# Kernel optimization log

Hardware: AMD Instinct MI355X
Metric: run time of the kernel (lower is better)

The kernel has to match this reference:

```python
import jax, jax.numpy as jnp
import numpy as np

BN = 1.0 / np.sqrt(1.0 + 1e-5)  # eval-mode BatchNorm at init (mean=0,var=1,gamma=1,beta=0)
EPS = 1e-5
WIN = 5
NH, HD = 8, 6

def _conv2d(x, w, ph, pw, groups=1):
    return jax.lax.conv_general_dilated(x, w, (1, 1), ((ph, ph), (pw, pw)),
        dimension_numbers=('NCHW', 'OIHW', 'NCHW'), feature_group_count=groups)

def _conv1d(x, w, p, groups=1):
    return jax.lax.conv_general_dilated(x, w, (1,), ((p, p),),
        dimension_numbers=('NCH', 'OIH', 'NCH'), feature_group_count=groups)

def _avgpool_t(x, k):
    s = jax.lax.reduce_window(x, 0.0, jax.lax.add, (1, 1, 1, k), (1, 1, 1, k), 'VALID')
    return s / k

def _ln(h, g, b):
    m = h.mean(-1, keepdims=True)
    v = h.var(-1, keepdims=True)  # biased, matches torch LayerNorm
    return (h - m) / jnp.sqrt(v + EPS) * g + b

def setup_inputs() -> dict:
    ks = jax.random.split(jax.random.key(0), 20)
    def n(i, shape, s=0.05):
        return jax.random.normal(ks[i], shape, dtype=jnp.float32) * s
    z = lambda *s: jnp.zeros(s, jnp.float32)
    o = lambda *s: jnp.ones(s, jnp.float32)
    return {
        'x': jax.random.normal(ks[0], (16, 1, 22, 16000), dtype=jnp.float32),
        'riem_w1': n(1, (253, 256)), 'riem_b1': z(256),
        'riem_w2': n(2, (256, 48)), 'riem_b2': z(48),
        'conv1_w': n(3, (16, 1, 1, 64)),
        'dw1_w': n(4, (32, 1, 22, 1)),
        'dw2_w': n(5, (32, 1, 1, 16)),
        'pw_w': n(6, (48, 32, 1, 1)),
        'tc1_w': n(7, (24, 2, 3)), 'tc1_b': z(24),
        'tc2_w': n(8, (48, 24, 1)), 'tc2_b': z(48),
        'fusion_proj': n(9, (48, 48), 0.15),
        'pos_enc': n(10, (1, 500, 48), 0.02),
        'ln1_g': o(4, 48), 'ln1_b': z(4, 48),
        'qkv_w': n(11, (4, 48, 144)), 'qkv_b': z(4, 144),
        'attn_proj_w': n(12, (4, 48, 48)), 'attn_proj_b': z(4, 48),
        'ln2_g': o(4, 48), 'ln2_b': z(4, 48),
        'ffn_w1': n(13, (4, 48, 192)), 'ffn_b1': z(4, 192),
        'ffn_w2': n(14, (4, 192, 48)), 'ffn_b2': z(4, 48),
        'cls_ln_g': o(48), 'cls_ln_b': z(48),
        'cls_w': n(15, (48, 4), 0.1), 'cls_b': z(4),
    }

def _forward(x, riem_w1, riem_b1, riem_w2, riem_b2, conv1_w, dw1_w, dw2_w, pw_w,
             tc1_w, tc1_b, tc2_w, tc2_b, fusion_proj, pos_enc,
             ln1_g, ln1_b, qkv_w, qkv_b, attn_proj_w, attn_proj_b,
             ln2_g, ln2_b, ffn_w1, ffn_b1, ffn_w2, ffn_b2,
             cls_ln_g, cls_ln_b, cls_w, cls_b):
    B = x.shape[0]
    # ---- Riemannian geometry branch ----
    xr = x[:, 0]                                   # (B, 22, T)
    C, T = xr.shape[1], xr.shape[2]
    xc = xr - xr.mean(-1, keepdims=True)
    cov = jnp.einsum('bct,bdt->bcd', xc, xc) / (T - 1)
    I = jnp.eye(C, dtype=x.dtype)
    cov = cov + I * 1e-5
    tr = jnp.trace(cov, axis1=1, axis2=2)
    cov = cov + I * (tr.mean() * 1e-3)
    L = jnp.linalg.cholesky(cov)
    dL = jnp.diagonal(L, axis1=-2, axis2=-1)
    log_cov = L * jnp.log(jnp.clip(dL, 1e-10))[:, None, :]   # L @ diag(log(diag L))
    iu = jnp.triu_indices(C)
    flat = log_cov[:, iu[0], iu[1]]                # (B, 253)
    r_feat = (jax.nn.elu(flat @ riem_w1 + riem_b1) @ riem_w2 + riem_b2)[:, None, :]
    # ---- Lightweight CNN branch (BatchNorms in eval = constant scale) ----
    h = _conv2d(x, conv1_w, 0, 32) * BN
    h = jax.nn.elu(_conv2d(h, dw1_w, 0, 0, groups=16) * BN)
    h = _avgpool_t(h, 8)
    h = _conv2d(h, dw2_w, 0, 8, groups=32) * BN
    h = jax.nn.elu(_conv2d(h, pw_w, 0, 0) * BN)
    h = _avgpool_t(h, 8)                            # (B, 48, 1, L)
    feat = jnp.transpose(h[:, :, 0, :], (0, 2, 1))  # (B, L, 48)
    t = _conv1d(jnp.transpose(feat, (0, 2, 1)), tc1_w, 1, groups=24) + tc1_b[None, :, None]
    t = jax.nn.gelu(t * BN, approximate=False)
    t = _conv1d(t, tc2_w, 0) + tc2_b[None, :, None]
    feat = feat + jnp.transpose(t, (0, 2, 1))
    # ---- Fusion + positional encoding ----
    fused = jnp.concatenate([r_feat, feat], axis=1) @ fusion_proj
    N = fused.shape[1]
    fused = fused + pos_enc[:, :N]
    # ---- Sparse (banded) transformer blocks ----
    idx = jnp.arange(N)
    band = jnp.abs(idx[:, None] - idx[None, :]) <= WIN   # allowed positions
    scale = HD ** -0.5
    for i in range(4):
        res = fused
        hh = _ln(fused, ln1_g[i], ln1_b[i])
        qkv = (hh @ qkv_w[i] + qkv_b[i]).reshape(B, N, 3, NH, HD)
        q = jnp.transpose(qkv[:, :, 0], (0, 2, 1, 3))
        k = jnp.transpose(qkv[:, :, 1], (0, 2, 1, 3))
        v = jnp.transpose(qkv[:, :, 2], (0, 2, 1, 3))
        att = jnp.einsum('bhqd,bhkd->bhqk', q, k) * scale
        att = jax.nn.softmax(jnp.where(band, att, -jnp.inf), axis=-1)
        o = jnp.einsum('bhqk,bhkd->bhqd', att, v)
        o = jnp.transpose(o, (0, 2, 1, 3)).reshape(B, N, NH * HD)
        fused = res + (o @ attn_proj_w[i] + attn_proj_b[i])
        res = fused
        hh = _ln(fused, ln2_g[i], ln2_b[i])
        hh = jax.nn.gelu(hh @ ffn_w1[i] + ffn_b1[i], approximate=False) @ ffn_w2[i] + ffn_b2[i]
        fused = res + hh
    g = fused.mean(axis=1)
    g = _ln(g, cls_ln_g, cls_ln_b)
    return g @ cls_w + cls_b

def reference(x, riem_w1, riem_b1, riem_w2, riem_b2, conv1_w, dw1_w, dw2_w, pw_w,
              tc1_w, tc1_b, tc2_w, tc2_b, fusion_proj, pos_enc,
              ln1_g, ln1_b, qkv_w, qkv_b, attn_proj_w, attn_proj_b,
              ln2_g, ln2_b, ffn_w1, ffn_b1, ffn_w2, ffn_b2,
              cls_ln_g, cls_ln_b, cls_w, cls_b):
    return _forward(x, riem_w1, riem_b1, riem_w2, riem_b2, conv1_w, dw1_w, dw2_w, pw_w,
                    tc1_w, tc1_b, tc2_w, tc2_b, fusion_proj, pos_enc,
                    ln1_g, ln1_b, qkv_w, qkv_b, attn_proj_w, attn_proj_b,
                    ln2_g, ln2_b, ffn_w1, ffn_b1, ffn_w2, ffn_b2,
                    cls_ln_g, cls_ln_b, cls_w, cls_b)
```

## Files before the change

### kernel.cpp

```cpp
#include <hip/hip_runtime.h>
#include <hip/hip_bf16.h>
#include <math.h>

#define BN_C 0.9999950000375f
#define NB 16
#define NC 22
#define NT 16000
#define NPAIR 253
#define NSEQ 251
#define ND 48
#define TR 8
#define TE 18

__device__ __forceinline__ unsigned short f2bf(float f) {
    union { float f; unsigned int u; } v; v.f = f;
    unsigned int r = v.u + 0x7fff + ((v.u >> 16) & 1);
    return (unsigned short)(r >> 16);
}
__device__ __forceinline__ float bf2f(unsigned short s) {
    union { unsigned int u; float f; } v; v.u = ((unsigned int)s) << 16;
    return v.f;
}

__global__ __launch_bounds__(256) void k_y(const float* __restrict__ x,
                                           const float* __restrict__ dw1,
                                           __hip_bfloat16* __restrict__ y) {
    int gid = blockIdx.x * 256 + threadIdx.x;
    int b = gid / 8000, tp = gid % 8000;
    int t = tp * 2;
    const float* xb = x + (size_t)b * NC * NT + t;
    float a0[32], a1[32];
    #pragma unroll
    for (int j = 0; j < 32; j++) { a0[j] = 0.f; a1[j] = 0.f; }
    for (int h = 0; h < NC; h++) {
        float2 xv = *(const float2*)&xb[(size_t)h * NT];
        #pragma unroll
        for (int j = 0; j < 32; j++) {
            float w = dw1[j * NC + h];
            a0[j] += w * xv.x; a1[j] += w * xv.y;
        }
    }
    unsigned int* yo = (unsigned int*)(y + (size_t)b * 32 * NT + t);
    #pragma unroll
    for (int j = 0; j < 32; j++) {
        unsigned int pk = (unsigned int)f2bf(a0[j]) | ((unsigned int)f2bf(a1[j]) << 16);
        yo[j * (NT / 2)] = pk;
    }
}

#define TCHUNK 500
#define XROW 504
__global__ __launch_bounds__(256) void k_covS(const float* __restrict__ x,
                                              float* __restrict__ covP,
                                              float* __restrict__ sumP) {
    int chunk = blockIdx.x, b = blockIdx.y;
    int t0 = chunk * TCHUNK;
    __shared__ unsigned short xs[NC * XROW];
    const float* xp = x + (size_t)b * NC * NT + t0;
    for (int i = threadIdx.x; i < NC * 126; i += 256) {
        int c = i / 126, q = i % 126;
        unsigned long long pk = 0ull;
        if (q < 125) {
            float4 v = *(const float4*)&xp[(size_t)c * NT + 4 * q];
            pk = (unsigned long long)f2bf(v.x) | ((unsigned long long)f2bf(v.y) << 16)
               | ((unsigned long long)f2bf(v.z) << 32) | ((unsigned long long)f2bf(v.w) << 48);
        }
        *(unsigned long long*)&xs[c * XROW + 4 * q] = pk;
    }
    __syncthreads();
    int p = threadIdx.x;
    if (p < NPAIR) {
        int c = 0, r = p;
        while (r >= NC - c) { r -= NC - c; c++; }
        int d = c + r;
        const unsigned short* xc = &xs[c * XROW];
        const unsigned short* xd = &xs[d * XROW];
        float a0 = 0, a1 = 0, a2 = 0, a3 = 0;
        float s0 = 0, s1 = 0, s2 = 0, s3 = 0;
        for (int t = 0; t < XROW; t += 8) {
            uint4 pc = *(const uint4*)&xc[t];
            uint4 pd = *(const uint4*)&xd[t];
            float c0 = bf2f((unsigned short)pc.x), c1 = bf2f((unsigned short)(pc.x >> 16));
            float c2 = bf2f((unsigned short)pc.y), c3 = bf2f((unsigned short)(pc.y >> 16));
            float c4 = bf2f((unsigned short)pc.z), c5 = bf2f((unsigned short)(pc.z >> 16));
            float c6 = bf2f((unsigned short)pc.w), c7 = bf2f((unsigned short)(pc.w >> 16));
            float d0 = bf2f((unsigned short)pd.x), d1 = bf2f((unsigned short)(pd.x >> 16));
            float d2 = bf2f((unsigned short)pd.y), d3 = bf2f((unsigned short)(pd.y >> 16));
            float d4 = bf2f((unsigned short)pd.z), d5 = bf2f((unsigned short)(pd.z >> 16));
            float d6 = bf2f((unsigned short)pd.w), d7 = bf2f((unsigned short)(pd.w >> 16));
            a0 += c0 * d0 + c4 * d4; a1 += c1 * d1 + c5 * d5;
            a2 += c2 * d2 + c6 * d6; a3 += c3 * d3 + c7 * d7;
            s0 += c0 + c4; s1 += c1 + c5; s2 += c2 + c6; s3 += c3 + c7;
        }
        covP[(size_t)chunk * NB * NPAIR + b * NPAIR + p] = (a0 + a1) + (a2 + a3);
        if (c == d) sumP[(size_t)chunk * NB * NC + b * NC + c] = (s0 + s1) + (s2 + s3);
    }
}

__global__ void k_cov_asm(const float* __restrict__ covP, const float* __restrict__ sumP,
                          float* __restrict__ cov, float* __restrict__ trb) {
    int b = blockIdx.x, t = threadIdx.x;
    __shared__ float ss[NC];
    __shared__ float red[256];
    if (t < NC) {
        float s = 0;
        for (int ch = 0; ch < 32; ch++) s += sumP[(size_t)ch * NB * NC + b * NC + t];
        ss[t] = s;
    }
    __syncthreads();
    float myTr = 0.f;
    if (t < NPAIR) {
        int c = 0, r = t;
        while (r >= NC - c) { r -= NC - c; c++; }
        int d = c + r;
        float v = 0;
        for (int ch = 0; ch < 32; ch++) v += covP[(size_t)ch * NB * NPAIR + b * NPAIR + t];
        v = (v - ss[c] * ss[d] / (float)NT) / (float)(NT - 1);
        if (c == d) { v += 1e-5f; myTr = v; }
        cov[b * 484 + c * NC + d] = v;
        cov[b * 484 + d * NC + c] = v;
    }
    red[t] = myTr;
    __syncthreads();
    for (int st = 128; st > 0; st >>= 1) {
        if (t < st) red[t] += red[t + st];
        __syncthreads();
    }
    if (t == 0) trb[b] = red[0];
}

__global__ __launch_bounds__(256) void k_cholfeat(
    const float* __restrict__ cov, const float* __restrict__ trb,
    const float* __restrict__ w1, const float* __restrict__ b1,
    const float* __restrict__ w2, const float* __restrict__ b2,
    float* __restrict__ rfeat) {
    int b = blockIdx.x, t = threadIdx.x;
    __shared__ float dvs[NC];
    __shared__ float hid[256];
    __shared__ float part[4][ND];
    if (t < 64) {
        int lane = t;
        float tv = (lane < NB) ? trb[lane] : 0.f;
        tv += __shfl_down(tv, 8, 16); tv += __shfl_down(tv, 4, 16);
        tv += __shfl_down(tv, 2, 16); tv += __shfl_down(tv, 1, 16);
        float trm = __shfl(tv, 0) * (0.001f / (float)NB);
        float a[NC];
        #pragma unroll
        for (int j = 0; j < NC; j++) {
            float v = (lane < NC) ? cov[b * 484 + lane * NC + j] : 0.f;
            a[j] = v + ((j == lane) ? trm : 0.f);
        }
        float diagv = 1.f;
        #pragma unroll
        for (int k = 0; k < NC; k++) {
            float akk = __shfl(a[k], k);
            float dk = sqrtf(akk);
            if (lane == k) { a[k] = dk; diagv = dk; }
            else if (lane > k) a[k] /= dk;
            float myak = a[k];
            #pragma unroll
            for (int j = k + 1; j < NC; j++) {
                float ljk = __shfl(myak, j);
                if (lane >= j) a[j] -= myak * ljk;
            }
        }
        if (lane < NC) dvs[lane] = diagv * logf(fmaxf(diagv, 1e-10f));
    }
    __syncthreads();
    {
        float acc = b1[t];
        #pragma unroll
        for (int d = 0; d < NC; d++) {
            int pos = d * NC - d * (d - 1) / 2;
            acc += dvs[d] * w1[pos * 256 + t];
        }
        hid[t] = (acc > 0.f) ? acc : expm1f(acc);
    }
    __syncthreads();
    if (t < 192) {
        int col = t % ND, kc = t / ND;
        float a = 0.f;
        #pragma unroll
        for (int i = 0; i < 64; i++) a += hid[kc * 64 + i] * w2[(kc * 64 + i) * ND + col];
        part[kc][col] = a;
    }
    __syncthreads();
    if (t < ND)
        rfeat[b * ND + t] = b2[t] + part[0][t] + part[1][t] + part[2][t] + part[3][t];
}

#define UT 256
__global__ __launch_bounds__(256) void k_conv64(const __hip_bfloat16* __restrict__ y,
                                                const float* __restrict__ c1w,
                                                float* __restrict__ p) {
    int tile = blockIdx.x, j = blockIdx.y, b = blockIdx.z;
    int u0 = tile * UT;
    __shared__ float yt[2376];
    const __hip_bfloat16* yp = y + ((size_t)(b * 32 + j)) * NT;
    int tbase = u0 * 8 - 32;
    for (int q = threadIdx.x; q < 1056; q += 256) {
        int i = 2 * q;
        int tq = tbase + i;
        float v0 = 0.f, v1 = 0.f;
        if (tq >= 0 && tq + 1 < NT) {
            unsigned int pk = *(const unsigned int*)(yp + tq);
            v0 = bf2f((unsigned short)pk); v1 = bf2f((unsigned short)(pk >> 16));
        } else {
            if (tq >= 0 && tq < NT) v0 = __bfloat162float(yp[tq]);
            if (tq + 1 >= 0 && tq + 1 < NT) v1 = __bfloat162float(yp[tq + 1]);
        }
        yt[i + (i >> 3)] = v0;
        int i1 = i + 1;
        yt[i1 + (i1 >> 3)] = v1;
    }
    __syncthreads();
    const float* cf = c1w + (j >> 1) * 64;
    int u = u0 + threadIdx.x;
    if (u < 2000) {
        int off = 8 * threadIdx.x;
        float acc[8];
        #pragma unroll
        for (int s = 0; s < 8; s++) acc[s] = 0.f;
        #pragma unroll
        for (int kb = 0; kb < 64; kb += 16) {
            float Yb[23];
            #pragma unroll
            for (int m = 0; m < 23; m++) {
                int idx = off + kb + m;
                Yb[m] = yt[idx + (idx >> 3)];
            }
            #pragma unroll
            for (int k = 0; k < 16; k++) {
                float c = cf[kb + k];
                #pragma unroll
                for (int s = 0; s < 8; s++) acc[s] += c * Yb[k + s];
            }
        }
        const float bn2 = BN_C * BN_C;
        float pv = 0.f;
        #pragma unroll
        for (int s = 0; s < 8; s++) {
            float z = bn2 * acc[s];
            pv += (z > 0.f) ? z : expm1f(z);
        }
        p[((size_t)(b * 32 + j)) * 2000 + u] = pv * 0.125f;
    }
}

__global__ __launch_bounds__(256) void k_stage2(const float* __restrict__ p,
                                                const float* __restrict__ dw2,
                                                const float* __restrict__ pw,
                                                float* __restrict__ feat) {
    int u2b = blockIdx.x * 4, b = blockIdx.y, t = threadIdx.x;
    __shared__ float pt[32][48];
    __shared__ float dval[32][32];
    __shared__ float w2s[512];
    __shared__ float pws[1536];
    for (int i = t; i < 512; i += 256) w2s[i] = dw2[i];
    for (int i = t; i < 1536; i += 256) pws[i] = pw[i];
    int base = 8 * u2b - 8;
    for (int i = t; i < 32 * 47; i += 256) {
        int j = i / 47, tt = i % 47;
        int gt = base + tt;
        pt[j][tt] = (gt >= 0 && gt < 2000) ? p[((size_t)(b * 32 + j)) * 2000 + gt] : 0.f;
    }
    __syncthreads();
    for (int i = t; i < 1024; i += 256) {
        int j = i >> 5, su = i & 31;
        int u = su >> 3, s = su & 7;
        float a = 0.f;
        #pragma unroll
        for (int k = 0; k < 16; k++) a += w2s[j * 16 + k] * pt[j][8 * u + s + k];
        dval[j][su] = a * BN_C;
    }
    __syncthreads();
    if (t < 192) {
        int col = t % ND, u = t / ND;
        int u2 = u2b + u;
        if (u2 < 250) {
            float wreg[32];
            #pragma unroll
            for (int j = 0; j < 32; j++) wreg[j] = pws[col * 32 + j];
            float acc = 0.f;
            #pragma unroll
            for (int s = 0; s < 8; s++) {
                float e = 0.f;
                #pragma unroll
                for (int j = 0; j < 32; j++) e += wreg[j] * dval[j][u * 8 + s];
                e *= BN_C;
                acc += (e > 0.f) ? e : expm1f(e);
            }
            feat[((size_t)b * 250 + u2) * ND + col] = acc * 0.125f;
        }
    }
}

__global__ __launch_bounds__(256) void k_fuse(
    const float* __restrict__ feat, const float* __restrict__ rfeat,
    const float* __restrict__ tc1w, const float* __restrict__ tc1b,
    const float* __restrict__ tc2w, const float* __restrict__ tc2b,
    const float* __restrict__ fp, const float* __restrict__ pe,
    float* __restrict__ fused) {
    int b = blockIdx.y;
    int sub = threadIdx.x >> 6, lt = threadIdx.x & 63;
    int n = blockIdx.x * 4 + sub;
    bool valid = (n < NSEQ);
    __shared__ float row[4][ND];
    __shared__ float g1[4][24];
    if (valid) {
        if (n == 0) {
            if (lt < ND) row[sub][lt] = rfeat[b * ND + lt];
        } else {
            int u = n - 1;
            if (lt < 24) {
                int m = lt;
                float a = tc1b[m];
                #pragma unroll
                for (int k = 0; k < 3; k++) {
                    int uu = u + k - 1;
                    if (uu >= 0 && uu < 250) {
                        float f0 = feat[((size_t)b * 250 + uu) * ND + 2 * m];
                        float f1 = feat[((size_t)b * 250 + uu) * ND + 2 * m + 1];
                        a += tc1w[m * 6 + k] * f0 + tc1w[m * 6 + 3 + k] * f1;
                    }
                }
                float z = a * BN_C;
                g1[sub][m] = 0.5f * z * (1.f + erff(z * 0.70710678f));
            }
        }
    }
    __syncthreads();
    if (valid && n > 0 && lt < ND) {
        int u = n - 1;
        float a = tc2b[lt];
        #pragma unroll
        for (int m = 0; m < 24; m++) a += tc2w[lt * 24 + m] * g1[sub][m];
        row[sub][lt] = feat[((size_t)b * 250 + u) * ND + lt] + a;
    }
    __syncthreads();
    if (valid && lt < ND) {
        float o = pe[n * ND + lt];
        for (int c = 0; c < ND; c++) o += row[sub][c] * fp[c * ND + lt];
        fused[((size_t)b * NSEQ + n) * ND + lt] = o;
    }
}

__global__ __launch_bounds__(512) void k_layer(
    float* __restrict__ fused,
    const float* __restrict__ g1v, const float* __restrict__ b1v,
    const float* __restrict__ qw, const float* __restrict__ qb,
    const float* __restrict__ apw, const float* __restrict__ apb,
    const float* __restrict__ g2v, const float* __restrict__ b2v,
    const float* __restrict__ w1, const float* __restrict__ fb1,
    const float* __restrict__ w2, const float* __restrict__ fb2) {
    int tile = blockIdx.x, b = blockIdx.y;
    int n0 = tile * TR;
    int t = threadIdx.x;
    __shared__ float row[TE][ND];
    __shared__ float hh[TE][ND];
    __shared__ float qkvS[TE * 144];
    __shared__ float ob[TR][ND];
    __shared__ float nrow[TR][ND];
    __shared__ float mrs[TE][2];
    __shared__ float part[4][TR][ND];
    float* hid = qkvS;

    for (int i = t; i < TE * ND; i += 512) {
        int e = i / ND, c = i % ND;
        int n = n0 - 5 + e;
        row[e][c] = (n >= 0 && n < NSEQ) ? fused[((size_t)b * NSEQ + n) * ND + c] : 0.f;
    }
    __syncthreads();
    if (t < TE * 16) {
        int r = t >> 4, i = t & 15;
        float v0 = row[r][i], v1 = row[r][i + 16], v2 = row[r][i + 32];
        float s = v0 + v1 + v2;
        s += __shfl_down(s, 8, 16); s += __shfl_down(s, 4, 16);
        s += __shfl_down(s, 2, 16); s += __shfl_down(s, 1, 16);
        float m = __shfl(s, 0, 16) * (1.f / ND);
        float d0 = v0 - m, d1 = v1 - m, d2 = v2 - m;
        float q = d0 * d0 + d1 * d1 + d2 * d2;
        q += __shfl_down(q, 8, 16); q += __shfl_down(q, 4, 16);
        q += __shfl_down(q, 2, 16); q += __shfl_down(q, 1, 16);
        if (i == 0) { mrs[r][0] = m; mrs[r][1] = rsqrtf(q * (1.f / ND) + 1e-5f); }
    }
    __syncthreads();
    for (int i = t; i < TE * ND; i += 512) {
        int e = i / ND, c = i % ND;
        hh[e][c] = (row[e][c] - mrs[e][0]) * mrs[e][1] * g1v[c] + b1v[c];
    }
    __syncthreads();
    if (t < 288) {
        int col = t % 144, eg = t / 144;
        float w[ND];
        #pragma unroll
        for (int c = 0; c < ND; c++) w[c] = qw[c * 144 + col];
        float bias = qb[col];
        for (int e = eg * 9; e < eg * 9 + 9; e++) {
            float a = bias;
            #pragma unroll
            for (int c = 0; c < ND; c++) a += hh[e][c] * w[c];
            qkvS[e * 144 + col] = a;
        }
    }
    __syncthreads();
    if (t < TR * 8) {
        int r = t >> 3, h = t & 7;
        int n = n0 + r;
        if (n < NSEQ) {
            int k0 = n - 5; if (k0 < 0) k0 = 0;
            int k1 = n + 5; if (k1 > NSEQ - 1) k1 = NSEQ - 1;
            int nk = k1 - k0 + 1;
            float q[6];
            #pragma unroll
            for (int d = 0; d < 6; d++) q[d] = qkvS[(r + 5) * 144 + h * 6 + d];
            float sc[11];
            float mx = -1e30f;
            for (int ki = 0; ki < nk; ki++) {
                int e = k0 + ki - n0 + 5;
                float s = 0;
                #pragma unroll
                for (int d = 0; d < 6; d++) s += q[d] * qkvS[e * 144 + 48 + h * 6 + d];
                s *= 0.4082482904638631f;
                sc[ki] = s; mx = fmaxf(mx, s);
            }
            float sum = 0;
            for (int ki = 0; ki < nk; ki++) { float e = expf(sc[ki] - mx); sc[ki] = e; sum += e; }
            float inv = 1.f / sum;
            float o[6] = {0, 0, 0, 0, 0, 0};
            for (int ki = 0; ki < nk; ki++) {
                int e = k0 + ki - n0 + 5;
                float pv = sc[ki] * inv;
                #pragma unroll
                for (int d = 0; d < 6; d++) o[d] += pv * qkvS[e * 144 + 96 + h * 6 + d];
            }
            #pragma unroll
            for (int d = 0; d < 6; d++) ob[r][h * 6 + d] = o[d];
        } else {
            #pragma unroll
            for (int d = 0; d < 6; d++) ob[r][h * 6 + d] = 0.f;
        }
    }
    __syncthreads();
    if (t < TR * ND) {
        int r = t / ND, col = t % ND;
        float a = apb[col];
        #pragma unroll
        for (int c = 0; c < ND; c++) a += ob[r][c] * apw[c * ND + col];
        nrow[r][col] = row[r + 5][col] + a;
    }
    __syncthreads();
    if (t < TR * 16) {
        int r = t >> 4, i = t & 15;
        float v0 = nrow[r][i], v1 = nrow[r][i + 16], v2 = nrow[r][i + 32];
        float s = v0 + v1 + v2;
        s += __shfl_down(s, 8, 16); s += __shfl_down(s, 4, 16);
        s += __shfl_down(s, 2, 16); s += __shfl_down(s, 1, 16);
        float m = __shfl(s, 0, 16) * (1.f / ND);
        float d0 = v0 - m, d1 = v1 - m, d2 = v2 - m;
        float q = d0 * d0 + d1 * d1 + d2 * d2;
        q += __shfl_down(q, 8, 16); q += __shfl_down(q, 4, 16);
        q += __shfl_down(q, 2, 16); q += __shfl_down(q, 1, 16);
        if (i == 0) { mrs[r][0] = m; mrs[r][1] = rsqrtf(q * (1.f / ND) + 1e-5f); }
    }
    __syncthreads();
    if (t < TR * ND) {
        int r = t / ND, c = t % ND;
        hh[r][c] = (nrow[r][c] - mrs[r][0]) * mrs[r][1] * g2v[c] + b2v[c];
    }
    __syncthreads();
    if (t < 384) {
        int col = t % 192, rg = t / 192;
        float w[ND];
        #pragma unroll
        for (int c = 0; c < ND; c++) w[c] = w1[c * 192 + col];
        float bias = fb1[col];
        for (int r = rg * 4; r < rg * 4 + 4; r++) {
            float a = bias;
            #pragma unroll
            for (int c = 0; c < ND; c++) a += hh[r][c] * w[c];
            hid[r * 192 + col] = 0.5f * a * (1.f + erff(a * 0.70710678f));
        }
    }
    __syncthreads();
    if (t < 384) {
        int col = t % ND, kc = (t / ND) & 3, rh = t / 192;
        float w[ND];
        #pragma unroll
        for (int i2 = 0; i2 < ND; i2++) w[i2] = w2[(kc * ND + i2) * ND + col];
        for (int r = rh * 4; r < rh * 4 + 4; r++) {
            float a = 0;
            #pragma unroll
            for (int i2 = 0; i2 < ND; i2++) a += hid[r * 192 + kc * ND + i2] * w[i2];
            part[kc][r][col] = a;
        }
    }
    __syncthreads();
    for (int i = t; i < TR * ND; i += 512) {
        int r = i / ND, c = i % ND;
        int n = n0 + r;
        if (n < NSEQ) {
            fused[((size_t)b * NSEQ + n) * ND + c] =
                nrow[r][c] + fb2[c] + part[0][r][c] + part[1][r][c] + part[2][r][c] + part[3][r][c];
        }
    }
}

__global__ void k_head(const float* __restrict__ fused, const float* __restrict__ lg,
                       const float* __restrict__ lb, const float* __restrict__ cw,
                       const float* __restrict__ cb, float* __restrict__ out) {
    int b = blockIdx.x, t = threadIdx.x;
    __shared__ float part[4][ND];
    __shared__ float gg[ND], mv[2];
    if (t < 192) {
        int col = t % ND, qt = t / ND;
        int nA = qt * 63;
        int nB = (nA + 63 < NSEQ) ? nA + 63 : NSEQ;
        float s = 0.f;
        for (int n = nA; n < nB; n++) s += fused[((size_t)b * NSEQ + n) * ND + col];
        part[qt][col] = s;
    }
    __syncthreads();
    if (t < ND) gg[t] = (part[0][t] + part[1][t] + part[2][t] + part[3][t]) * (1.f / NSEQ);
    __syncthreads();
    if (t == 0) {
        float m = 0;
        for (int c = 0; c < ND; c++) m += gg[c];
        m /= (float)ND;
        float v = 0;
        for (int c = 0; c < ND; c++) { float dd = gg[c] - m; v += dd * dd; }
        v /= (float)ND;
        mv[0] = m; mv[1] = rsqrtf(v + 1e-5f);
    }
    __syncthreads();
    if (t < ND) gg[t] = (gg[t] - mv[0]) * mv[1] * lg[t] + lb[t];
    __syncthreads();
    if (t < 4) {
        float a = cb[t];
        for (int c = 0; c < ND; c++) a += gg[c] * cw[c * 4 + t];
        out[b * 4 + t] = a;
    }
}

extern "C" void kernel_launch(void* const* d_in, const int* in_sizes, int n_in,
                              void* d_out, int out_size, void* d_ws, size_t ws_size,
                              hipStream_t stream) {
    const float* x       = (const float*)d_in[0];
    const float* riem_w1 = (const float*)d_in[1];
    const float* riem_b1 = (const float*)d_in[2];
    const float* riem_w2 = (const float*)d_in[3];
    const float* riem_b2 = (const float*)d_in[4];
    const float* conv1_w = (const float*)d_in[5];
    const float* dw1_w   = (const float*)d_in[6];
    const float* dw2_w   = (const float*)d_in[7];
    const float* pw_w    = (const float*)d_in[8];
    const float* tc1_w   = (const float*)d_in[9];
    const float* tc1_b   = (const float*)d_in[10];
    const float* tc2_w   = (const float*)d_in[11];
    const float* tc2_b   = (const float*)d_in[12];
    const float* fusion  = (const float*)d_in[13];
    const float* pos_enc = (const float*)d_in[14];
    const float* ln1_g   = (const float*)d_in[15];
    const float* ln1_b   = (const float*)d_in[16];
    const float* qkv_w   = (const float*)d_in[17];
    const float* qkv_b   = (const float*)d_in[18];
    const float* apw     = (const float*)d_in[19];
    const float* apb     = (const float*)d_in[20];
    const float* ln2_g   = (const float*)d_in[21];
    const float* ln2_b   = (const float*)d_in[22];
    const float* ffn_w1  = (const float*)d_in[23];
    const float* ffn_b1  = (const float*)d_in[24];
    const float* ffn_w2  = (const float*)d_in[25];
    const float* ffn_b2  = (const float*)d_in[26];
    const float* cls_g   = (const float*)d_in[27];
    const float* cls_b_  = (const float*)d_in[28];
    const float* cls_w   = (const float*)d_in[29];
    const float* cls_bb  = (const float*)d_in[30];
    float* out = (float*)d_out;

    float* ws = (float*)d_ws;
    float* covP  = ws;
    float* sumP  = ws + 129536;
    float* trb   = ws + 140800;
    float* cov   = ws + 140816;
    float* rfeat = ws + 148560;
    float* feat  = ws + 149328;
    float* fused = ws + 341328;
    float* pbuf  = ws + 534096;
    __hip_bfloat16* ybuf = (__hip_bfloat16*)(ws + 1558096);

    k_y<<<500, 256, 0, stream>>>(x, dw1_w, ybuf);
    k_covS<<<dim3(32, NB), 256, 0, stream>>>(x, covP, sumP);
    k_cov_asm<<<NB, 256, 0, stream>>>(covP, sumP, cov, trb);
    k_cholfeat<<<NB, 256, 0, stream>>>(cov, trb, riem_w1, riem_b1, riem_w2, riem_b2, rfeat);

    k_conv64<<<dim3(8, 32, NB), 256, 0, stream>>>(ybuf, conv1_w, pbuf);
    k_stage2<<<dim3(63, NB), 256, 0, stream>>>(pbuf, dw2_w, pw_w, feat);
    k_fuse<<<dim3(63, NB), 256, 0, stream>>>(feat, rfeat, tc1_w, tc1_b, tc2_w, tc2_b,
                                             fusion, pos_enc, fused);

    for (int i = 0; i < 4; i++) {
        k_layer<<<dim3(32, NB), 512, 0, stream>>>(
            fused, ln1_g + i * 48, ln1_b + i * 48, qkv_w + i * 6912, qkv_b + i * 144,
            apw + i * 2304, apb + i * 48, ln2_g + i * 48, ln2_b + i * 48,
            ffn_w1 + i * 9216, ffn_b1 + i * 192, ffn_w2 + i * 9216, ffn_b2 + i * 48);
    }

    k_head<<<NB, 256, 0, stream>>>(fused, cls_g, cls_b_, cls_w, cls_bb, out);
}
```

Before: 294.6 us.

## Fuse covariance assembly into Cholesky and stage2 into fuse; widen conv64 tiles

Folds covariance assembly and the trace reduction into the Cholesky-feature kernel. Each block recomputes the cross-batch trace from the partial sums, so no separate kernel or global round trip is needed. Merges stage2 and the fuse kernel: each block computes a 6-row halo of features in shared memory instead of writing and rereading a feature buffer. Doubles conv64 outputs per thread, halving the block count, to improve register reuse of the loaded inputs. These remove two launches and some global traffic, at the cost of redundant halo and trace work plus higher register pressure in conv64.

```diff
diff --git a/kernel.cpp b/kernel.cpp
--- a/kernel.cpp
+++ b/kernel.cpp
@@ -97,57 +97,55 @@
     }
 }
 
-__global__ void k_cov_asm(const float* __restrict__ covP, const float* __restrict__ sumP,
-                          float* __restrict__ cov, float* __restrict__ trb) {
+__global__ __launch_bounds__(256) void k_cholfeat(
+    const float* __restrict__ covP, const float* __restrict__ sumP,
+    const float* __restrict__ w1, const float* __restrict__ b1,
+    const float* __restrict__ w2, const float* __restrict__ b2,
+    float* __restrict__ rfeat) {
     int b = blockIdx.x, t = threadIdx.x;
-    __shared__ float ss[NC];
-    __shared__ float red[256];
-    if (t < NC) {
-        float s = 0;
-        for (int ch = 0; ch < 32; ch++) s += sumP[(size_t)ch * NB * NC + b * NC + t];
-        ss[t] = s;
-    }
-    __syncthreads();
-    float myTr = 0.f;
+    __shared__ float ssA[NB][NC];
+    __shared__ float covL[484];
+    __shared__ float trS[NB];
+    __shared__ float dvs[NC];
+    __shared__ float hid[256];
+    __shared__ float part[4][ND];
+    if (t < NB) trS[t] = 0.f;
+    for (int i = t; i < NB * NC; i += 256) {
+        int bb = i / NC, c = i % NC;
+        float s = 0.f;
+        for (int ch = 0; ch < 32; ch++) s += sumP[(size_t)ch * NB * NC + bb * NC + c];
+        ssA[bb][c] = s;
+    }
+    __syncthreads();
     if (t < NPAIR) {
         int c = 0, r = t;
         while (r >= NC - c) { r -= NC - c; c++; }
         int d = c + r;
-        float v = 0;
+        float v = 0.f;
         for (int ch = 0; ch < 32; ch++) v += covP[(size_t)ch * NB * NPAIR + b * NPAIR + t];
-        v = (v - ss[c] * ss[d] / (float)NT) / (float)(NT - 1);
-        if (c == d) { v += 1e-5f; myTr = v; }
-        cov[b * 484 + c * NC + d] = v;
-        cov[b * 484 + d * NC + c] = v;
-    }
-    red[t] = myTr;
-    __syncthreads();
-    for (int st = 128; st > 0; st >>= 1) {
-        if (t < st) red[t] += red[t + st];
-        __syncthreads();
-    }
-    if (t == 0) trb[b] = red[0];
-}
-
-__global__ __launch_bounds__(256) void k_cholfeat(
-    const float* __restrict__ cov, const float* __restrict__ trb,
-    const float* __restrict__ w1, const float* __restrict__ b1,
-    const float* __restrict__ w2, const float* __restrict__ b2,
-    float* __restrict__ rfeat) {
-    int b = blockIdx.x, t = threadIdx.x;
-    __shared__ float dvs[NC];
-    __shared__ float hid[256];
-    __shared__ float part[4][ND];
+        v = (v - ssA[b][c] * ssA[b][d] / (float)NT) / (float)(NT - 1);
+        if (c == d) v += 1e-5f;
+        covL[c * NC + d] = v;
+        covL[d * NC + c] = v;
+    }
+    for (int i = t; i < NB * NC; i += 256) {
+        int bb = i / NC, c = i % NC;
+        int pos = c * NC - c * (c - 1) / 2;
+        float v = 0.f;
+        for (int ch = 0; ch < 32; ch++) v += covP[(size_t)ch * NB * NPAIR + bb * NPAIR + pos];
+        v = (v - ssA[bb][c] * ssA[bb][c] / (float)NT) / (float)(NT - 1) + 1e-5f;
+        atomicAdd(&trS[bb], v);
+    }
+    __syncthreads();
+    float trs = 0.f;
+    for (int i = 0; i < NB; i++) trs += trS[i];
+    float trm = trs * (0.001f / (float)NB);
     if (t < 64) {
         int lane = t;
-        float tv = (lane < NB) ? trb[lane] : 0.f;
-        tv += __shfl_down(tv, 8, 16); tv += __shfl_down(tv, 4, 16);
-        tv += __shfl_down(tv, 2, 16); tv += __shfl_down(tv, 1, 16);
-        float trm = __shfl(tv, 0) * (0.001f / (float)NB);
         float a[NC];
         #pragma unroll
         for (int j = 0; j < NC; j++) {
-            float v = (lane < NC) ? cov[b * 484 + lane * NC + j] : 0.f;
+            float v = (lane < NC) ? covL[lane * NC + j] : 0.f;
             a[j] = v + ((j == lane) ? trm : 0.f);
         }
         float diagv = 1.f;
@@ -189,16 +187,16 @@
         rfeat[b * ND + t] = b2[t] + part[0][t] + part[1][t] + part[2][t] + part[3][t];
 }
 
-#define UT 256
+#define CT2 512
 __global__ __launch_bounds__(256) void k_conv64(const __hip_bfloat16* __restrict__ y,
                                                 const float* __restrict__ c1w,
                                                 float* __restrict__ p) {
     int tile = blockIdx.x, j = blockIdx.y, b = blockIdx.z;
-    int u0 = tile * UT;
-    __shared__ float yt[2376];
+    int u0 = tile * CT2;
+    __shared__ float yt[4680];
     const __hip_bfloat16* yp = y + ((size_t)(b * 32 + j)) * NT;
     int tbase = u0 * 8 - 32;
-    for (int q = threadIdx.x; q < 1056; q += 256) {
+    for (int q = threadIdx.x; q < 2080; q += 256) {
         int i = 2 * q;
         int tq = tbase + i;
         float v0 = 0.f, v1 = 0.f;
@@ -215,133 +213,135 @@
     }
     __syncthreads();
     const float* cf = c1w + (j >> 1) * 64;
-    int u = u0 + threadIdx.x;
+    int u = u0 + 2 * threadIdx.x;
     if (u < 2000) {
-        int off = 8 * threadIdx.x;
-        float acc[8];
-        #pragma unroll
-        for (int s = 0; s < 8; s++) acc[s] = 0.f;
+        int off = 16 * threadIdx.x;
+        float acc[16];
+        #pragma unroll
+        for (int s = 0; s < 16; s++) acc[s] = 0.f;
         #pragma unroll
         for (int kb = 0; kb < 64; kb += 16) {
-            float Yb[23];
-            #pragma unroll
-            for (int m = 0; m < 23; m++) {
+            float Y[31];
+            #pragma unroll
+            for (int m = 0; m < 31; m++) {
                 int idx = off + kb + m;
-                Yb[m] = yt[idx + (idx >> 3)];
+                Y[m] = yt[idx + (idx >> 3)];
             }
             #pragma unroll
             for (int k = 0; k < 16; k++) {
                 float c = cf[kb + k];
                 #pragma unroll
-                for (int s = 0; s < 8; s++) acc[s] += c * Yb[k + s];
+                for (int s = 0; s < 16; s++) acc[s] += c * Y[k + s];
             }
         }
         const float bn2 = BN_C * BN_C;
-        float pv = 0.f;
+        float pv0 = 0.f, pv1 = 0.f;
         #pragma unroll
         for (int s = 0; s < 8; s++) {
-            float z = bn2 * acc[s];
-            pv += (z > 0.f) ? z : expm1f(z);
-        }
-        p[((size_t)(b * 32 + j)) * 2000 + u] = pv * 0.125f;
-    }
-}
-
-__global__ __launch_bounds__(256) void k_stage2(const float* __restrict__ p,
-                                                const float* __restrict__ dw2,
-                                                const float* __restrict__ pw,
-                                                float* __restrict__ feat) {
-    int u2b = blockIdx.x * 4, b = blockIdx.y, t = threadIdx.x;
-    __shared__ float pt[32][48];
-    __shared__ float dval[32][32];
-    __shared__ float w2s[512];
-    __shared__ float pws[1536];
-    for (int i = t; i < 512; i += 256) w2s[i] = dw2[i];
-    for (int i = t; i < 1536; i += 256) pws[i] = pw[i];
-    int base = 8 * u2b - 8;
-    for (int i = t; i < 32 * 47; i += 256) {
-        int j = i / 47, tt = i % 47;
-        int gt = base + tt;
-        pt[j][tt] = (gt >= 0 && gt < 2000) ? p[((size_t)(b * 32 + j)) * 2000 + gt] : 0.f;
-    }
-    __syncthreads();
-    for (int i = t; i < 1024; i += 256) {
-        int j = i >> 5, su = i & 31;
-        int u = su >> 3, s = su & 7;
-        float a = 0.f;
-        #pragma unroll
-        for (int k = 0; k < 16; k++) a += w2s[j * 16 + k] * pt[j][8 * u + s + k];
-        dval[j][su] = a * BN_C;
-    }
-    __syncthreads();
-    if (t < 192) {
-        int col = t % ND, u = t / ND;
-        int u2 = u2b + u;
-        if (u2 < 250) {
-            float wreg[32];
-            #pragma unroll
-            for (int j = 0; j < 32; j++) wreg[j] = pws[col * 32 + j];
-            float acc = 0.f;
-            #pragma unroll
-            for (int s = 0; s < 8; s++) {
-                float e = 0.f;
-                #pragma unroll
-                for (int j = 0; j < 32; j++) e += wreg[j] * dval[j][u * 8 + s];
-                e *= BN_C;
-                acc += (e > 0.f) ? e : expm1f(e);
-            }
-            feat[((size_t)b * 250 + u2) * ND + col] = acc * 0.125f;
-        }
-    }
-}
-
-__global__ __launch_bounds__(256) void k_fuse(
-    const float* __restrict__ feat, const float* __restrict__ rfeat,
+            float z0 = bn2 * acc[s];
+            pv0 += (z0 > 0.f) ? z0 : expm1f(z0);
+            float z1 = bn2 * acc[8 + s];
+            pv1 += (z1 > 0.f) ? z1 : expm1f(z1);
+        }
+        size_t base = ((size_t)(b * 32 + j)) * 2000;
+        p[base + u] = pv0 * 0.125f;
+        if (u + 1 < 2000) p[base + u + 1] = pv1 * 0.125f;
+    }
+}
+
+__global__ __launch_bounds__(256) void k_stage2fuse(
+    const float* __restrict__ p, const float* __restrict__ dw2,
+    const float* __restrict__ pw, const float* __restrict__ rfeat,
     const float* __restrict__ tc1w, const float* __restrict__ tc1b,
     const float* __restrict__ tc2w, const float* __restrict__ tc2b,
     const float* __restrict__ fp, const float* __restrict__ pe,
     float* __restrict__ fused) {
-    int b = blockIdx.y;
-    int sub = threadIdx.x >> 6, lt = threadIdx.x & 63;
-    int n = blockIdx.x * 4 + sub;
-    bool valid = (n < NSEQ);
+    int bx = blockIdx.x, b = blockIdx.y, t = threadIdx.x;
+    __shared__ float pt[32][64];
+    __shared__ float dval[32][48];
+    __shared__ float feat6[6][ND];
+    __shared__ float w2s[512];
+    __shared__ float pws[1536];
+    __shared__ float g1[4][24];
     __shared__ float row[4][ND];
-    __shared__ float g1[4][24];
-    if (valid) {
-        if (n == 0) {
-            if (lt < ND) row[sub][lt] = rfeat[b * ND + lt];
-        } else {
-            int u = n - 1;
-            if (lt < 24) {
-                int m = lt;
-                float a = tc1b[m];
+    for (int i = t; i < 512; i += 256) w2s[i] = dw2[i];
+    for (int i = t; i < 1536; i += 256) pws[i] = pw[i];
+    int gt0 = 32 * bx - 24;
+    for (int i = t; i < 32 * 63; i += 256) {
+        int j = i / 63, tt = i % 63;
+        int gt = gt0 + tt;
+        pt[j][tt] = (gt >= 0 && gt < 2000) ? p[((size_t)(b * 32 + j)) * 2000 + gt] : 0.f;
+    }
+    __syncthreads();
+    for (int i = t; i < 1536; i += 256) {
+        int j = i / 48, su = i % 48;
+        int w = su >> 3, s = su & 7;
+        float a = 0.f;
+        #pragma unroll
+        for (int k = 0; k < 16; k++) a += w2s[j * 16 + k] * pt[j][8 * w + s + k];
+        dval[j][su] = a * BN_C;
+    }
+    __syncthreads();
+    for (int i = t; i < 6 * ND; i += 256) {
+        int w = i / ND, col = i % ND;
+        int u2 = 4 * bx - 2 + w;
+        float acc = 0.f;
+        if (u2 >= 0 && u2 < 250) {
+            float wreg[32];
+            #pragma unroll
+            for (int j = 0; j < 32; j++) wreg[j] = pws[col * 32 + j];
+            #pragma unroll
+            for (int s = 0; s < 8; s++) {
+                float e = 0.f;
                 #pragma unroll
-                for (int k = 0; k < 3; k++) {
-                    int uu = u + k - 1;
-                    if (uu >= 0 && uu < 250) {
-                        float f0 = feat[((size_t)b * 250 + uu) * ND + 2 * m];
-                        float f1 = feat[((size_t)b * 250 + uu) * ND + 2 * m + 1];
-                        a += tc1w[m * 6 + k] * f0 + tc1w[m * 6 + 3 + k] * f1;
-                    }
-                }
-                float z = a * BN_C;
-                g1[sub][m] = 0.5f * z * (1.f + erff(z * 0.70710678f));
-            }
-        }
-    }
-    __syncthreads();
-    if (valid && n > 0 && lt < ND) {
-        int u = n - 1;
-        float a = tc2b[lt];
-        #pragma unroll
-        for (int m = 0; m < 24; m++) a += tc2w[lt * 24 + m] * g1[sub][m];
-        row[sub][lt] = feat[((size_t)b * 250 + u) * ND + lt] + a;
-    }
-    __syncthreads();
-    if (valid && lt < ND) {
-        float o = pe[n * ND + lt];
-        for (int c = 0; c < ND; c++) o += row[sub][c] * fp[c * ND + lt];
-        fused[((size_t)b * NSEQ + n) * ND + lt] = o;
+                for (int j = 0; j < 32; j++) e += wreg[j] * dval[j][w * 8 + s];
+                e *= BN_C;
+                acc += (e > 0.f) ? e : expm1f(e);
+            }
+            acc *= 0.125f;
+        }
+        feat6[w][col] = acc;
+    }
+    __syncthreads();
+    if (t < 96) {
+        int sub = t / 24, m = t % 24;
+        int n = 4 * bx + sub;
+        if (n >= 1 && n < NSEQ) {
+            float a = tc1b[m];
+            #pragma unroll
+            for (int k = 0; k < 3; k++) {
+                int w = sub + k;
+                a += tc1w[m * 6 + k] * feat6[w][2 * m]
+                   + tc1w[m * 6 + 3 + k] * feat6[w][2 * m + 1];
+            }
+            float z = a * BN_C;
+            g1[sub][m] = 0.5f * z * (1.f + erff(z * 0.70710678f));
+        }
+    }
+    __syncthreads();
+    if (t < 192) {
+        int sub = t / ND, col = t % ND;
+        int n = 4 * bx + sub;
+        if (n < NSEQ) {
+            if (n == 0) {
+                row[sub][col] = rfeat[b * ND + col];
+            } else {
+                float a = tc2b[col];
+                #pragma unroll
+                for (int m = 0; m < 24; m++) a += tc2w[col * 24 + m] * g1[sub][m];
+                row[sub][col] = feat6[sub + 1][col] + a;
+            }
+        }
+    }
+    __syncthreads();
+    if (t < 192) {
+        int sub = t / ND, col = t % ND;
+        int n = 4 * bx + sub;
+        if (n < NSEQ) {
+            float o = pe[n * ND + col];
+            for (int c = 0; c < ND; c++) o += row[sub][c] * fp[c * ND + col];
+            fused[((size_t)b * NSEQ + n) * ND + col] = o;
+        }
     }
 }
 
@@ -581,23 +581,19 @@
     float* ws = (float*)d_ws;
     float* covP  = ws;
     float* sumP  = ws + 129536;
-    float* trb   = ws + 140800;
-    float* cov   = ws + 140816;
-    float* rfeat = ws + 148560;
-    float* feat  = ws + 149328;
-    float* fused = ws + 341328;
-    float* pbuf  = ws + 534096;
-    __hip_bfloat16* ybuf = (__hip_bfloat16*)(ws + 1558096);
+    float* rfeat = ws + 140800;
+    float* fused = ws + 141568;
+    float* pbuf  = ws + 334336;
+    __hip_bfloat16* ybuf = (__hip_bfloat16*)(ws + 1358336);
 
     k_y<<<500, 256, 0, stream>>>(x, dw1_w, ybuf);
     k_covS<<<dim3(32, NB), 256, 0, stream>>>(x, covP, sumP);
-    k_cov_asm<<<NB, 256, 0, stream>>>(covP, sumP, cov, trb);
-    k_cholfeat<<<NB, 256, 0, stream>>>(cov, trb, riem_w1, riem_b1, riem_w2, riem_b2, rfeat);
-
-    k_conv64<<<dim3(8, 32, NB), 256, 0, stream>>>(ybuf, conv1_w, pbuf);
-    k_stage2<<<dim3(63, NB), 256, 0, stream>>>(pbuf, dw2_w, pw_w, feat);
-    k_fuse<<<dim3(63, NB), 256, 0, stream>>>(feat, rfeat, tc1_w, tc1_b, tc2_w, tc2_b,
-                                             fusion, pos_enc, fused);
+    k_cholfeat<<<NB, 256, 0, stream>>>(covP, sumP, riem_w1, riem_b1, riem_w2, riem_b2, rfeat);
+
+    k_conv64<<<dim3(4, 32, NB), 256, 0, stream>>>(ybuf, conv1_w, pbuf);
+    k_stage2fuse<<<dim3(63, NB), 256, 0, stream>>>(pbuf, dw2_w, pw_w, rfeat,
+                                                   tc1_w, tc1_b, tc2_w, tc2_b,
+                                                   fusion, pos_enc, fused);
 
     for (int i = 0; i < 4; i++) {
         k_layer<<<dim3(32, NB), 512, 0, stream>>>(
```

Measured after the change: 302.3 us. 2.6% more time.
